# Kernel tuning notes

Measured on AMD Instinct MI355X. Metric: run time of the kernel, lower is better.

## Reference

```python
import jax, jax.numpy as jnp
import numpy as np

H = 768


def lstm_cell(x, h, c, Wih, Whh, b):
    # PyTorch LSTMCell gate order: i, f, g, o
    gates = x @ Wih.T + h @ Whh.T + b
    i, f, g, o = jnp.split(gates, 4, axis=-1)
    c = jax.nn.sigmoid(f) * c + jax.nn.sigmoid(i) * jnp.tanh(g)
    h = jax.nn.sigmoid(o) * jnp.tanh(c)
    return h, c


def run_lstm(x, Wih, Whh, b, reverse):
    B = x.shape[0]
    Hd = Whh.shape[1]
    def step(carry, xt):
        h, c = lstm_cell(xt, carry[0], carry[1], Wih, Whh, b)
        return (h, c), h
    init = (jnp.zeros((B, Hd), x.dtype), jnp.zeros((B, Hd), x.dtype))
    _, hs = jax.lax.scan(step, init, jnp.swapaxes(x, 0, 1), reverse=reverse)
    return jnp.swapaxes(hs, 0, 1)


def _forward(hidden_state, golds, lstm_Wih_f, lstm_Whh_f, lstm_b_f,
             lstm_Wih_b, lstm_Whh_b, lstm_b_b, subw_Wih, subw_Whh, subw_b,
             word_Wih, word_Whh, word_b, cls_W, cls_b):
    B, T, _ = hidden_state.shape
    dt = hidden_state.dtype
    out_f = run_lstm(hidden_state, lstm_Wih_f, lstm_Whh_f, lstm_b_f, False)
    out_b = run_lstm(hidden_state, lstm_Wih_b, lstm_Whh_b, lstm_b_b, True)
    lstm_out = jnp.concatenate([out_f, out_b], -1)  # [B, T, 2H]

    subw_map = jnp.array([1, 2, 2], dtype=jnp.int32)
    word_map = jnp.array([0, 1, 1], dtype=jnp.int32)
    bidx = jnp.arange(B)
    S1, S2 = 2 * T + 2, T + 1
    carry0 = (jnp.zeros((S1, B, H), dt), jnp.zeros((S1, B, H), dt), jnp.zeros((B,), jnp.int32),
              jnp.zeros((S2, B, H), dt), jnp.zeros((S2, B, H), dt), jnp.zeros((B,), jnp.int32))
    xs = (jnp.swapaxes(lstm_out[:, :T - 1], 0, 1),  # features for subword cell at step idx-1
          jnp.swapaxes(lstm_out[:, 1:T], 0, 1),     # features concatenated into cls at step idx
          golds[:, 1:T].T.astype(jnp.int32))

    def step(carry, x):
        sh, sc, spos, wh, wc, wpos = carry
        x_prev, x_cur, g = x
        # subword stack-LSTM: read top-of-stack state, push new state at pos+1
        h1, c1 = lstm_cell(x_prev, sh[spos, bidx], sc[spos, bidx], subw_Wih, subw_Whh, subw_b)
        sh = sh.at[spos + 1, bidx].set(h1)
        sc = sc.at[spos + 1, bidx].set(c1)
        subword = jnp.concatenate([h1, c1], -1)  # [B, 2H] input to word stack-LSTM
        # word stack-LSTM
        h2, c2 = lstm_cell(subword, wh[wpos, bidx], wc[wpos, bidx], word_Wih, word_Whh, word_b)
        wh = wh.at[wpos + 1, bidx].set(h2)
        wc = wc.at[wpos + 1, bidx].set(c2)
        out = jnp.concatenate([h2, x_cur], -1) @ cls_W.T + cls_b  # [B, 2]
        # training path: ops from gold actions
        sop = subw_map[g]
        wop = word_map[g]
        spos = jnp.where(sop == 1, spos + 1, 0)      # APP: push; SEP: clear subword stack
        wpos = jnp.where(wop == 1, wpos + 1, wpos)   # SEP: push word; APP: hold
        return (sh, sc, spos, wh, wc, wpos), out

    _, outs = jax.lax.scan(step, carry0, xs)  # [T-1, B, 2]
    pred0 = jnp.broadcast_to(jnp.asarray([-1.0, 1.0], dt), (1, B, 2))
    return jnp.swapaxes(jnp.concatenate([pred0, outs], 0), 0, 1)  # [B, T, 2]


def setup_inputs() -> dict:
    key = jax.random.key(0)
    ks = jax.random.split(key, 12)
    B, T = 64, 256
    s = 0.02
    W = lambda k, shape: jax.random.normal(k, shape, jnp.float32) * s
    return {
        "hidden_state": jax.random.normal(ks[0], (B, T, H), jnp.float32),
        "golds": jax.random.randint(ks[1], (B, T), 0, 2),
        "lstm_Wih_f": W(ks[2], (4 * H, H)), "lstm_Whh_f": W(ks[3], (4 * H, H)), "lstm_b_f": jnp.zeros((4 * H,), jnp.float32),
        "lstm_Wih_b": W(ks[4], (4 * H, H)), "lstm_Whh_b": W(ks[5], (4 * H, H)), "lstm_b_b": jnp.zeros((4 * H,), jnp.float32),
        "subw_Wih": W(ks[6], (4 * H, 2 * H)), "subw_Whh": W(ks[7], (4 * H, H)), "subw_b": jnp.zeros((4 * H,), jnp.float32),
        "word_Wih": W(ks[8], (4 * H, 2 * H)), "word_Whh": W(ks[9], (4 * H, H)), "word_b": jnp.zeros((4 * H,), jnp.float32),
        "cls_W": W(ks[10], (2, 3 * H)), "cls_b": jnp.zeros((2,), jnp.float32),
    }


def reference(hidden_state, golds, lstm_Wih_f, lstm_Whh_f, lstm_b_f,
              lstm_Wih_b, lstm_Whh_b, lstm_b_b, subw_Wih, subw_Whh, subw_b,
              word_Wih, word_Whh, word_b, cls_W, cls_b):
    return _forward(hidden_state, golds, lstm_Wih_f, lstm_Whh_f, lstm_b_f,
                    lstm_Wih_b, lstm_Whh_b, lstm_b_b, subw_Wih, subw_Whh, subw_b,
                    word_Wih, word_Whh, word_b, cls_W, cls_b)
```

## Files before the change

kernel.cpp:

```cpp
#include <hip/hip_runtime.h>
#include <hip/hip_bf16.h>

typedef __attribute__((ext_vector_type(8))) short bf16x8;
typedef __attribute__((ext_vector_type(4))) float f32x4;
typedef __attribute__((ext_vector_type(4))) unsigned u32x4;

#define HD   768
#define NB   64
#define NT   256
#define NGATE 3072
#define FPAD 32

__device__ __forceinline__ float fast_sig(float x) { return 1.f / (1.f + __expf(-x)); }
__device__ __forceinline__ float fast_tanh(float x) {
  float t = __expf(-2.f * fabsf(x));
  float r = (1.f - t) / (1.f + t);
  return x < 0.f ? -r : r;
}
__device__ __forceinline__ float bf2f(unsigned short u) {
  union { unsigned i; float f; } v; v.i = ((unsigned)u) << 16; return v.f;
}
__device__ __forceinline__ unsigned short f2bfu(float f) {
  union { __hip_bfloat16 b; unsigned short u; } c;
  c.b = __float2bfloat16(f);
  return c.u;
}
__device__ __forceinline__ unsigned pack2(float a, float b) {
  return (unsigned)f2bfu(a) | ((unsigned)f2bfu(b) << 16);
}

__device__ __forceinline__ int aload(int* p) {
  return __hip_atomic_load(p, __ATOMIC_RELAXED, __HIP_MEMORY_SCOPE_AGENT);
}
__device__ __forceinline__ void ustore(unsigned* p, unsigned v) {
  __hip_atomic_store(p, v, __ATOMIC_RELAXED, __HIP_MEMORY_SCOPE_AGENT);
}
__device__ __forceinline__ u32x4 cload16(const char* p) {
  u32x4 r;
  asm volatile("global_load_dwordx4 %0, %1, off sc0 sc1"
               : "=v"(r) : "v"(p) : "memory");
  return r;
}

__device__ __forceinline__ void arrive_flag(int* f) {
  asm volatile("s_waitcnt vmcnt(0)" ::: "memory");
  __syncthreads();
  if (threadIdx.x == 0)
    __hip_atomic_fetch_add(f, 1, __ATOMIC_RELAXED, __HIP_MEMORY_SCOPE_AGENT);
}

__device__ __forceinline__ void wait2(int* fa, int ta, int* fb, int tb) {
  int tid = threadIdx.x;
  int* p = nullptr; int tgt = 0;
  if (tid < 96)                            { p = fa + tid * FPAD;         tgt = ta; }
  else if (fb && tid >= 128 && tid < 224)  { p = fb + (tid - 128) * FPAD; tgt = tb; }
  if (p && tgt > 0) {
    int guard = 0;
    while (aload(p) < tgt) {
      __builtin_amdgcn_s_sleep(1);
      if (++guard > (1 << 17)) break;
    }
  }
  __syncthreads();
}

__device__ __forceinline__ int frag_dw(int b, int j) {
  return (((((j >> 5) * 4 + (b >> 4)) * 4 + ((j >> 3) & 3)) * 16 + (b & 15)) * 4)
         + ((j & 7) >> 1);
}

__device__ __forceinline__ int wswz(int r) {
  return ((r & 7) << 4) | (((r >> 3) & 3) << 7);
}

__device__ __forceinline__ void load_W_lds(unsigned short* Wl,
                                           const __hip_bfloat16* Wg,
                                           int n_base, int K)
{
  int chunksPerRow = (K * 2) / 16;
  int total = 32 * chunksPerRow;
  for (int idx = threadIdx.x; idx < total; idx += 256) {
    int r  = idx / chunksPerRow;
    int cb = (idx % chunksPerRow) * 16;
    bf16x8 v = *(const bf16x8*)((const char*)(Wg + (long)(n_base + r) * K) + cb);
    *(bf16x8*)((char*)Wl + (long)r * (K * 2) + (cb ^ wswz(r))) = v;
  }
}

__device__ __forceinline__ void mfma_cached(
    const __hip_bfloat16* a0p, int NIT,
    const char* w0, const char* w1, int xr0, int xr1, int kk,
    f32x4& acc0, f32x4& acc1)
{
  #pragma unroll 4
  for (int it = 0; it < NIT; ++it) {
    bf16x8 av = *(const bf16x8*)(a0p + it * 32 + kk);
    int oo = (it * 32 + kk) * 2;
    bf16x8 bv0 = *(const bf16x8*)(w0 + (oo ^ xr0));
    bf16x8 bv1 = *(const bf16x8*)(w1 + (oo ^ xr1));
    acc0 = __builtin_amdgcn_mfma_f32_16x16x32_bf16(av, bv0, acc0, 0, 0, 0);
    acc1 = __builtin_amdgcn_mfma_f32_16x16x32_bf16(av, bv1, acc1, 0, 0, 0);
  }
}

template<int CF>
__device__ __forceinline__ void mfma_frag(
    const char* Fbase, int l, int w,
    const char* w0, const char* w1, int xr0, int xr1, int kk, int kbase,
    f32x4& acc0, f32x4& acc1)
{
  const char* fp = Fbase + (size_t)(w * 64 + l) * 16;
  u32x4 st[2][12];
  #pragma unroll
  for (int i = 0; i < 12; ++i)
    st[0][i] = cload16(fp + (size_t)i * 4096);
  #pragma unroll
  for (int c = 0; c < CF / 12; ++c) {
    if (c + 1 < CF / 12) {
      #pragma unroll
      for (int i = 0; i < 12; ++i)
        st[(c + 1) & 1][i] = cload16(fp + (size_t)((c + 1) * 12 + i) * 4096);
      asm volatile("s_waitcnt vmcnt(12)" ::: "memory");
    } else {
      asm volatile("s_waitcnt vmcnt(0)" ::: "memory");
    }
    __builtin_amdgcn_sched_barrier(0);
    #pragma unroll
    for (int i = 0; i < 12; ++i) {
      int oo = ((kbase + c * 12 + i) * 32 + kk) * 2;
      bf16x8 av = __builtin_bit_cast(bf16x8, st[c & 1][i]);
      bf16x8 bv0 = *(const bf16x8*)(w0 + (oo ^ xr0));
      bf16x8 bv1 = *(const bf16x8*)(w1 + (oo ^ xr1));
      acc0 = __builtin_amdgcn_mfma_f32_16x16x32_bf16(av, bv0, acc0, 0, 0, 0);
      acc1 = __builtin_amdgcn_mfma_f32_16x16x32_bf16(av, bv1, acc1, 0, 0, 0);
    }
  }
}

__device__ __forceinline__ void pack_seg(const float* Wih, const float* Whh,
                                         __hip_bfloat16* dst, int Kih,
                                         long id0, long stride)
{
  int K = Kih + HD;
  long total = (long)NGATE * K;
  for (long idx = id0; idx < total; idx += stride) {
    int np = (int)(idx / K), k = (int)(idx % K);
    int j = np >> 2, g = np & 3;
    int n = g * HD + j;
    float v = (k < Kih) ? Wih[(long)n * Kih + k] : Whh[(long)n * HD + (k - Kih)];
    dst[idx] = __float2bfloat16(v);
  }
}

__global__ void setup_kernel(
    const float* __restrict__ x,
    const float* __restrict__ WihF, const float* __restrict__ WhhF,
    const float* __restrict__ WihB, const float* __restrict__ WhhB,
    const float* __restrict__ WihS, const float* __restrict__ WhhS,
    const float* __restrict__ WihW, const float* __restrict__ WhhW,
    __hip_bfloat16* __restrict__ X16,
    __hip_bfloat16* __restrict__ WF, __hip_bfloat16* __restrict__ WB,
    __hip_bfloat16* __restrict__ WS, __hip_bfloat16* __restrict__ WW)
{
  long id0 = (long)blockIdx.x * blockDim.x + threadIdx.x;
  long stride = (long)gridDim.x * blockDim.x;
  for (long i = id0; i < (long)NB * NT * HD; i += stride)
    X16[i] = __float2bfloat16(x[i]);
  pack_seg(WihF, WhhF, WF, 768, id0, stride);
  pack_seg(WihB, WhhB, WB, 768, id0, stride);
  pack_seg(WihS, WhhS, WS, 1536, id0, stride);
  pack_seg(WihW, WhhW, WW, 1536, id0, stride);
}

__global__ void fill_sentinel(float* out, int n, float v)
{
  int i = blockIdx.x * blockDim.x + threadIdx.x;
  if (i < n) out[i] = v;
}

__global__ __launch_bounds__(256, 1) void bilstm_persist(
    const __hip_bfloat16* __restrict__ X16,
    const __hip_bfloat16* __restrict__ WF,
    const __hip_bfloat16* __restrict__ WB,
    const float* __restrict__ bF, const float* __restrict__ bB,
    unsigned* __restrict__ H16u,
    __hip_bfloat16* __restrict__ L16,
    int* __restrict__ flags)
{
  __shared__ unsigned short Wl[32 * 1536];
  __shared__ float gl[64][33];
  int blk = blockIdx.x, dir = blk / 96, nt = blk % 96;
  load_W_lds(Wl, dir ? WB : WF, nt * 32, 1536);
  const float* bias = dir ? bB : bF;
  int* myflags = flags + dir * 96 * FPAD;
  int tid = threadIdx.x;
  unsigned* L16u = (unsigned*)L16;

  int w = tid >> 6, l = tid & 63, lr = l & 15, lh = l >> 4;
  const char* w0 = (const char*)Wl + lr * 3072;
  const char* w1 = (const char*)Wl + (16 + lr) * 3072;
  int xr0 = wswz(lr), xr1 = wswz(16 + lr);
  int kk = 8 * lh;
  int bA = 16 * w + lr;

  int e0 = tid * 2;
  int b = e0 >> 3, jj = e0 & 7;
  int j0 = nt * 8 + jj;
  float bv[2][4];
  #pragma unroll
  for (int u = 0; u < 2; ++u) {
    bv[u][0] = bias[j0 + u];          bv[u][1] = bias[HD + j0 + u];
    bv[u][2] = bias[2 * HD + j0 + u]; bv[u][3] = bias[3 * HD + j0 + u];
  }
  int fdw = frag_dw(b, j0);
  float cst[2] = {0.f, 0.f};
  __syncthreads();

  for (int s = 0; s < NT; ++s) {
    int par = s & 1;
    int t = dir ? (NT - 1 - s) : s;
    f32x4 acc0 = {0.f, 0.f, 0.f, 0.f};
    f32x4 acc1 = {0.f, 0.f, 0.f, 0.f};
    mfma_cached(X16 + (long)t * HD + (long)bA * (NT * HD), 24,
                w0, w1, xr0, xr1, kk, acc0, acc1);
    if (s > 0) wait2(myflags, s, nullptr, 0);
    mfma_frag<24>((const char*)(H16u + (long)(par * 2 + dir) * 24576),
                  l, w, w0, w1, xr0, xr1, kk, 24, acc0, acc1);
    #pragma unroll
    for (int r = 0; r < 4; ++r) {
      gl[16 * w + 4 * lh + r][lr]      = acc0[r];
      gl[16 * w + 4 * lh + r][16 + lr] = acc1[r];
    }
    __syncthreads();
    float hv[2];
    #pragma unroll
    for (int u = 0; u < 2; ++u) {
      int col = 4 * (jj + u);
      float vi = gl[b][col + 0] + bv[u][0];
      float vf = gl[b][col + 1] + bv[u][1];
      float vg = gl[b][col + 2] + bv[u][2];
      float vo = gl[b][col + 3] + bv[u][3];
      float si = fast_sig(vi), sf = fast_sig(vf), so = fast_sig(vo);
      float tg = fast_tanh(vg);
      float c = sf * cst[u] + si * tg;
      cst[u] = c;
      hv[u] = so * fast_tanh(c);
    }
    unsigned pk = pack2(hv[0], hv[1]);
    ustore(H16u + (long)((par ^ 1) * 2 + dir) * 24576 + fdw, pk);
    L16u[((long)b * NT + t) * 768 + dir * 384 + (j0 >> 1)] = pk;
    if (s < NT - 1) arrive_flag(myflags + nt * FPAD);
  }
}

__global__ __launch_bounds__(256) void clsx_kernel(
    const __hip_bfloat16* __restrict__ L16,
    const float* __restrict__ clsW, const float* __restrict__ clsb,
    float* __restrict__ out)
{
  int t = blockIdx.x;
  int tid = threadIdx.x;
  if (tid >= 128) return;
  int b = tid >> 1, o = tid & 1;
  if (t == 0) {
    out[((long)b * NT) * 2 + o] = o ? 1.f : -1.f;
    return;
  }
  const bf16x8* xp = (const bf16x8*)(L16 + ((long)b * NT + t) * 1536);
  const float* w = clsW + o * 2304 + HD;
  float s = clsb[o];
  for (int k = 0; k < 192; ++k) {
    bf16x8 v = xp[k];
    #pragma unroll
    for (int e = 0; e < 8; ++e)
      s += bf2f((unsigned short)v[e]) * w[k * 8 + e];
  }
  out[((long)b * NT + t) * 2 + o] = s;
}

__global__ __launch_bounds__(256, 1) void stack_persist(
    const __hip_bfloat16* __restrict__ L16,
    const __hip_bfloat16* __restrict__ WS,
    const __hip_bfloat16* __restrict__ WW,
    const float* __restrict__ bS, const float* __restrict__ bW,
    const int* __restrict__ golds,
    const float* __restrict__ clsW,
    unsigned* __restrict__ H1Su,
    unsigned* __restrict__ H2Su,
    unsigned* __restrict__ SUBWu,
    float* __restrict__ out,
    int* __restrict__ flags)
{
  __shared__ unsigned short Wl[32 * 2304];
  __shared__ float gl[64][33];
  int blk = blockIdx.x, role = blk / 96, nt = blk % 96;
  int* flagS = flags + 2 * 96 * FPAD;
  int* flagW = flags + 3 * 96 * FPAD;
  const float* bias = role ? bW : bS;
  load_W_lds(Wl, role ? WW : WS, nt * 32, 2304);
  int tid = threadIdx.x;

  int w = tid >> 6, l = tid & 63, lr = l & 15, lh = l >> 4;
  const char* w0 = (const char*)Wl + lr * 4608;
  const char* w1 = (const char*)Wl + (16 + lr) * 4608;
  int xr0 = wswz(lr), xr1 = wswz(16 + lr);
  int kk = 8 * lh;
  int bA = 16 * w + lr;

  int e0 = tid * 2;
  int b = e0 >> 3, jj = e0 & 7;
  int j0 = nt * 8 + jj;
  float bv[2][4];
  #pragma unroll
  for (int u = 0; u < 2; ++u) {
    bv[u][0] = bias[j0 + u];          bv[u][1] = bias[HD + j0 + u];
    bv[u][2] = bias[2 * HD + j0 + u]; bv[u][3] = bias[3 * HD + j0 + u];
  }
  const int* gp = golds + b * NT + 1;
  int fdw_h = frag_dw(b, j0);
  float cst[2] = {0.f, 0.f};
  float hreg[2] = {0.f, 0.f};
  __syncthreads();

  if (role == 0) {
    int fdw_c = frag_dw(b, 768 + j0);
    for (int s = 0; s < NT - 1; ++s) {
      f32x4 acc0 = {0.f, 0.f, 0.f, 0.f};
      f32x4 acc1 = {0.f, 0.f, 0.f, 0.f};
      mfma_cached(L16 + (long)s * 1536 + (long)bA * (NT * 1536), 48,
                  w0, w1, xr0, xr1, kk, acc0, acc1);
      wait2(flagS, s, flagW, s - 3);
      mfma_frag<24>((const char*)(H1Su + (long)(s & 1) * 24576),
                    l, w, w0, w1, xr0, xr1, kk, 48, acc0, acc1);
      #pragma unroll
      for (int r = 0; r < 4; ++r) {
        gl[16 * w + 4 * lh + r][lr]      = acc0[r];
        gl[16 * w + 4 * lh + r][16 + lr] = acc1[r];
      }
      __syncthreads();
      float h1v[2], c1v[2];
      #pragma unroll
      for (int u = 0; u < 2; ++u) {
        int col = 4 * (jj + u);
        float vi = gl[b][col + 0] + bv[u][0];
        float vf = gl[b][col + 1] + bv[u][1];
        float vg = gl[b][col + 2] + bv[u][2];
        float vo = gl[b][col + 3] + bv[u][3];
        float si = fast_sig(vi), sf = fast_sig(vf), so = fast_sig(vo);
        float tg = fast_tanh(vg);
        c1v[u] = sf * cst[u] + si * tg;
        h1v[u] = so * fast_tanh(c1v[u]);
      }
      int g = gp[s];
      bool push = (g == 0);
      unsigned pkh = pack2(h1v[0], h1v[1]);
      unsigned pkc = pack2(c1v[0], c1v[1]);
      unsigned* sb = SUBWu + (long)(s & 3) * 49152;
      ustore(sb + fdw_h, pkh);
      ustore(sb + fdw_c, pkc);
      ustore(H1Su + (long)((s + 1) & 1) * 24576 + fdw_h, push ? pkh : 0u);
      cst[0] = push ? c1v[0] : 0.f;
      cst[1] = push ? c1v[1] : 0.f;
      arrive_flag(flagS + nt * FPAD);
    }
  } else {
    float cw0[2], cw1[2];
    #pragma unroll
    for (int u = 0; u < 2; ++u) { cw0[u] = clsW[j0 + u]; cw1[u] = clsW[2304 + j0 + u]; }
    for (int s = 0; s < NT - 1; ++s) {
      wait2(flagW, s, nullptr, 0);
      f32x4 acc0 = {0.f, 0.f, 0.f, 0.f};
      f32x4 acc1 = {0.f, 0.f, 0.f, 0.f};
      mfma_frag<24>((const char*)(H2Su + (long)(s & 1) * 24576),
                    l, w, w0, w1, xr0, xr1, kk, 48, acc0, acc1);
      wait2(flagS, s + 1, nullptr, 0);
      mfma_frag<48>((const char*)(SUBWu + (long)(s & 3) * 49152),
                    l, w, w0, w1, xr0, xr1, kk, 0, acc0, acc1);
      #pragma unroll
      for (int r = 0; r < 4; ++r) {
        gl[16 * w + 4 * lh + r][lr]      = acc0[r];
        gl[16 * w + 4 * lh + r][16 + lr] = acc1[r];
      }
      __syncthreads();
      float p0 = 0.f, p1 = 0.f;
      float h2v[2], c2v[2];
      #pragma unroll
      for (int u = 0; u < 2; ++u) {
        int col = 4 * (jj + u);
        float vi = gl[b][col + 0] + bv[u][0];
        float vf = gl[b][col + 1] + bv[u][1];
        float vg = gl[b][col + 2] + bv[u][2];
        float vo = gl[b][col + 3] + bv[u][3];
        float si = fast_sig(vi), sf = fast_sig(vf), so = fast_sig(vo);
        float tg = fast_tanh(vg);
        c2v[u] = sf * cst[u] + si * tg;
        h2v[u] = so * fast_tanh(c2v[u]);
        p0 += h2v[u] * cw0[u];
        p1 += h2v[u] * cw1[u];
      }
      int g = gp[s];
      bool push = (g >= 1);
      #pragma unroll
      for (int u = 0; u < 2; ++u) {
        cst[u]  = push ? c2v[u] : cst[u];
        hreg[u] = push ? h2v[u] : hreg[u];
      }
      ustore(H2Su + (long)((s + 1) & 1) * 24576 + fdw_h, pack2(hreg[0], hreg[1]));
      p0 += __shfl_down(p0, 1); p1 += __shfl_down(p1, 1);
      p0 += __shfl_down(p0, 2); p1 += __shfl_down(p1, 2);
      if ((tid & 3) == 0) {
        int bb = tid >> 2;
        atomicAdd(&out[((long)bb * NT + s + 1) * 2 + 0], p0);
        atomicAdd(&out[((long)bb * NT + s + 1) * 2 + 1], p1);
      }
      if (s < NT - 2) arrive_flag(flagW + nt * FPAD);
    }
  }
}

extern "C" void kernel_launch(void* const* d_in, const int* in_sizes, int n_in,
                              void* d_out, int out_size, void* d_ws, size_t ws_size,
                              hipStream_t stream)
{
  const float* x     = (const float*)d_in[0];
  const int*   golds = (const int*)d_in[1];
  const float* WihF  = (const float*)d_in[2];
  const float* WhhF  = (const float*)d_in[3];
  const float* bF    = (const float*)d_in[4];
  const float* WihB  = (const float*)d_in[5];
  const float* WhhB  = (const float*)d_in[6];
  const float* bB    = (const float*)d_in[7];
  const float* WihS  = (const float*)d_in[8];
  const float* WhhS  = (const float*)d_in[9];
  const float* bS    = (const float*)d_in[10];
  const float* WihW  = (const float*)d_in[11];
  const float* WhhW  = (const float*)d_in[12];
  const float* bW    = (const float*)d_in[13];
  const float* clsW  = (const float*)d_in[14];
  const float* clsb  = (const float*)d_in[15];
  float* out = (float*)d_out;

  const size_t OFF_X16  = 0;
  const size_t OFF_WF   = 25165824;
  const size_t OFF_WB   = 34603008;
  const size_t OFF_WS   = 44040192;
  const size_t OFF_WW   = 58195968;
  const size_t OFF_L16  = 72351744;
  const size_t OFF_H16  = 122683392;
  const size_t OFF_H1S  = 123076608;
  const size_t OFF_H2S  = 123273216;
  const size_t OFF_SUBW = 123469824;
  const size_t OFF_FLG  = 124256256;
  const size_t WS_NEEDED = 124305408;

  if (ws_size < WS_NEEDED) {
    fill_sentinel<<<(out_size + 255) / 256, 256, 0, stream>>>(out, out_size, 12345.f);
    return;
  }

  char* ws = (char*)d_ws;
  __hip_bfloat16* X16  = (__hip_bfloat16*)(ws + OFF_X16);
  __hip_bfloat16* WF   = (__hip_bfloat16*)(ws + OFF_WF);
  __hip_bfloat16* WB   = (__hip_bfloat16*)(ws + OFF_WB);
  __hip_bfloat16* WSp  = (__hip_bfloat16*)(ws + OFF_WS);
  __hip_bfloat16* WWp  = (__hip_bfloat16*)(ws + OFF_WW);
  __hip_bfloat16* L16  = (__hip_bfloat16*)(ws + OFF_L16);
  unsigned*       H16u = (unsigned*)(ws + OFF_H16);
  unsigned*       H1Su = (unsigned*)(ws + OFF_H1S);
  unsigned*       H2Su = (unsigned*)(ws + OFF_H2S);
  unsigned*       SUBWu= (unsigned*)(ws + OFF_SUBW);
  int*            flags= (int*)(ws + OFF_FLG);

  setup_kernel<<<4096, 256, 0, stream>>>(x, WihF, WhhF, WihB, WhhB,
                                         WihS, WhhS, WihW, WhhW,
                                         X16, WF, WB, WSp, WWp);
  hipMemsetAsync(ws + OFF_H16, 0, WS_NEEDED - OFF_H16, stream);

  bilstm_persist<<<192, 256, 0, stream>>>(X16, WF, WB, bF, bB, H16u, L16, flags);

  clsx_kernel<<<NT, 256, 0, stream>>>(L16, clsW, clsb, out);

  stack_persist<<<192, 256, 0, stream>>>(L16, WSp, WWp, bS, bW, golds, clsW,
                                         H1Su, H2Su, SUBWu, out, flags);
}
```

Baseline: 4.056 ms.

## Overlap recurrent-state fragment loads with input-projection MFMAs and deepen load pipelining

The bidirectional LSTM and subword-cell loops now split the cached input-projection MFMA work in half. They issue all 24 coherent loads of the recurrent h fragment right after the flag wait, then run the second half of the input MFMAs while those loads are in flight. The word-cell loop issues the H2 loads before waiting on the subword flag and keeps three 12-load groups in flight with explicit vmcnt waits, instead of running two sequential double-buffered fragment passes. The classifier kernel now uses all 256 threads, with each pair splitting the dot product, and gold reads are hoisted. The cost is higher register pressure from more buffered fragments, plus reliance on hand-counted vmcnt values.

New measurement: 4.145 ms (median of 2 runs). 1.02x slower.

```diff
diff --git a/kernel.cpp b/kernel.cpp
--- a/kernel.cpp
+++ b/kernel.cpp
@@ -28,6 +28,9 @@
 __device__ __forceinline__ unsigned pack2(float a, float b) {
   return (unsigned)f2bfu(a) | ((unsigned)f2bfu(b) << 16);
 }
+
+#define VMW(N) do { asm volatile("s_waitcnt vmcnt(" #N ")" ::: "memory"); \
+                    __builtin_amdgcn_sched_barrier(0); } while (0)
 
 __device__ __forceinline__ int aload(int* p) {
   return __hip_atomic_load(p, __ATOMIC_RELAXED, __HIP_MEMORY_SCOPE_AGENT);
@@ -88,12 +91,12 @@
 }
 
 __device__ __forceinline__ void mfma_cached(
-    const __hip_bfloat16* a0p, int NIT,
+    const __hip_bfloat16* a0p, int kbase, int NIT,
     const char* w0, const char* w1, int xr0, int xr1, int kk,
     f32x4& acc0, f32x4& acc1)
 {
   #pragma unroll 4
-  for (int it = 0; it < NIT; ++it) {
+  for (int it = kbase; it < kbase + NIT; ++it) {
     bf16x8 av = *(const bf16x8*)(a0p + it * 32 + kk);
     int oo = (it * 32 + kk) * 2;
     bf16x8 bv0 = *(const bf16x8*)(w0 + (oo ^ xr0));
@@ -103,37 +106,25 @@
   }
 }
 
-template<int CF>
-__device__ __forceinline__ void mfma_frag(
-    const char* Fbase, int l, int w,
-    const char* w0, const char* w1, int xr0, int xr1, int kk, int kbase,
-    f32x4& acc0, f32x4& acc1)
-{
-  const char* fp = Fbase + (size_t)(w * 64 + l) * 16;
-  u32x4 st[2][12];
+__device__ __forceinline__ void issue12(u32x4* dst, const char* base, int c0) {
   #pragma unroll
   for (int i = 0; i < 12; ++i)
-    st[0][i] = cload16(fp + (size_t)i * 4096);
+    dst[i] = cload16(base + (size_t)(c0 + i) * 4096);
+}
+
+__device__ __forceinline__ void mfma_st12(
+    const u32x4* st, int kbase,
+    const char* w0, const char* w1, int xr0, int xr1, int kk,
+    f32x4& acc0, f32x4& acc1)
+{
   #pragma unroll
-  for (int c = 0; c < CF / 12; ++c) {
-    if (c + 1 < CF / 12) {
-      #pragma unroll
-      for (int i = 0; i < 12; ++i)
-        st[(c + 1) & 1][i] = cload16(fp + (size_t)((c + 1) * 12 + i) * 4096);
-      asm volatile("s_waitcnt vmcnt(12)" ::: "memory");
-    } else {
-      asm volatile("s_waitcnt vmcnt(0)" ::: "memory");
-    }
-    __builtin_amdgcn_sched_barrier(0);
-    #pragma unroll
-    for (int i = 0; i < 12; ++i) {
-      int oo = ((kbase + c * 12 + i) * 32 + kk) * 2;
-      bf16x8 av = __builtin_bit_cast(bf16x8, st[c & 1][i]);
-      bf16x8 bv0 = *(const bf16x8*)(w0 + (oo ^ xr0));
-      bf16x8 bv1 = *(const bf16x8*)(w1 + (oo ^ xr1));
-      acc0 = __builtin_amdgcn_mfma_f32_16x16x32_bf16(av, bv0, acc0, 0, 0, 0);
-      acc1 = __builtin_amdgcn_mfma_f32_16x16x32_bf16(av, bv1, acc1, 0, 0, 0);
-    }
+  for (int i = 0; i < 12; ++i) {
+    int oo = ((kbase + i) * 32 + kk) * 2;
+    bf16x8 av = __builtin_bit_cast(bf16x8, st[i]);
+    bf16x8 bv0 = *(const bf16x8*)(w0 + (oo ^ xr0));
+    bf16x8 bv1 = *(const bf16x8*)(w1 + (oo ^ xr1));
+    acc0 = __builtin_amdgcn_mfma_f32_16x16x32_bf16(av, bv0, acc0, 0, 0, 0);
+    acc1 = __builtin_amdgcn_mfma_f32_16x16x32_bf16(av, bv1, acc1, 0, 0, 0);
   }
 }
 
@@ -219,13 +210,20 @@
   for (int s = 0; s < NT; ++s) {
     int par = s & 1;
     int t = dir ? (NT - 1 - s) : s;
+    const __hip_bfloat16* xb = X16 + (long)t * HD + (long)bA * (NT * HD);
     f32x4 acc0 = {0.f, 0.f, 0.f, 0.f};
     f32x4 acc1 = {0.f, 0.f, 0.f, 0.f};
-    mfma_cached(X16 + (long)t * HD + (long)bA * (NT * HD), 24,
-                w0, w1, xr0, xr1, kk, acc0, acc1);
+    mfma_cached(xb, 0, 12, w0, w1, xr0, xr1, kk, acc0, acc1);
     if (s > 0) wait2(myflags, s, nullptr, 0);
-    mfma_frag<24>((const char*)(H16u + (long)(par * 2 + dir) * 24576),
-                  l, w, w0, w1, xr0, xr1, kk, 24, acc0, acc1);
+    const char* fpH = (const char*)(H16u + (long)(par * 2 + dir) * 24576)
+                      + (size_t)(w * 64 + l) * 16;
+    u32x4 hA[12], hB[12];
+    issue12(hA, fpH, 0);
+    issue12(hB, fpH, 12);
+    mfma_cached(xb, 12, 12, w0, w1, xr0, xr1, kk, acc0, acc1);
+    VMW(0);
+    mfma_st12(hA, 24, w0, w1, xr0, xr1, kk, acc0, acc1);
+    mfma_st12(hB, 36, w0, w1, xr0, xr1, kk, acc0, acc1);
     #pragma unroll
     for (int r = 0; r < 4; ++r) {
       gl[16 * w + 4 * lh + r][lr]      = acc0[r];
@@ -260,22 +258,22 @@
 {
   int t = blockIdx.x;
   int tid = threadIdx.x;
-  if (tid >= 128) return;
-  int b = tid >> 1, o = tid & 1;
+  int b = tid >> 2, o = (tid >> 1) & 1, hh = tid & 1;
   if (t == 0) {
-    out[((long)b * NT) * 2 + o] = o ? 1.f : -1.f;
+    if (hh == 0) out[((long)b * NT) * 2 + o] = o ? 1.f : -1.f;
     return;
   }
-  const bf16x8* xp = (const bf16x8*)(L16 + ((long)b * NT + t) * 1536);
-  const float* w = clsW + o * 2304 + HD;
-  float s = clsb[o];
-  for (int k = 0; k < 192; ++k) {
+  const bf16x8* xp = (const bf16x8*)(L16 + ((long)b * NT + t) * 1536 + hh * 768);
+  const float* wv = clsW + o * 2304 + HD + hh * 768;
+  float s = 0.f;
+  for (int k = 0; k < 96; ++k) {
     bf16x8 v = xp[k];
     #pragma unroll
     for (int e = 0; e < 8; ++e)
-      s += bf2f((unsigned short)v[e]) * w[k * 8 + e];
-  }
-  out[((long)b * NT + t) * 2 + o] = s;
+      s += bf2f((unsigned short)v[e]) * wv[k * 8 + e];
+  }
+  s += __shfl_down(s, 1);
+  if (hh == 0) out[((long)b * NT + t) * 2 + o] = s + clsb[o];
 }
 
 __global__ __launch_bounds__(256, 1) void stack_persist(
@@ -325,13 +323,21 @@
   if (role == 0) {
     int fdw_c = frag_dw(b, 768 + j0);
     for (int s = 0; s < NT - 1; ++s) {
+      int g = gp[s];
+      const __hip_bfloat16* lb = L16 + (long)s * 1536 + (long)bA * (NT * 1536);
       f32x4 acc0 = {0.f, 0.f, 0.f, 0.f};
       f32x4 acc1 = {0.f, 0.f, 0.f, 0.f};
-      mfma_cached(L16 + (long)s * 1536 + (long)bA * (NT * 1536), 48,
-                  w0, w1, xr0, xr1, kk, acc0, acc1);
+      mfma_cached(lb, 0, 24, w0, w1, xr0, xr1, kk, acc0, acc1);
       wait2(flagS, s, flagW, s - 3);
-      mfma_frag<24>((const char*)(H1Su + (long)(s & 1) * 24576),
-                    l, w, w0, w1, xr0, xr1, kk, 48, acc0, acc1);
+      const char* fpH1 = (const char*)(H1Su + (long)(s & 1) * 24576)
+                         + (size_t)(w * 64 + l) * 16;
+      u32x4 hA[12], hB[12];
+      issue12(hA, fpH1, 0);
+      issue12(hB, fpH1, 12);
+      mfma_cached(lb, 24, 24, w0, w1, xr0, xr1, kk, acc0, acc1);
+      VMW(0);
+      mfma_st12(hA, 48, w0, w1, xr0, xr1, kk, acc0, acc1);
+      mfma_st12(hB, 60, w0, w1, xr0, xr1, kk, acc0, acc1);
       #pragma unroll
       for (int r = 0; r < 4; ++r) {
         gl[16 * w + 4 * lh + r][lr]      = acc0[r];
@@ -351,7 +357,6 @@
         c1v[u] = sf * cst[u] + si * tg;
         h1v[u] = so * fast_tanh(c1v[u]);
       }
-      int g = gp[s];
       bool push = (g == 0);
       unsigned pkh = pack2(h1v[0], h1v[1]);
       unsigned pkc = pack2(c1v[0], c1v[1]);
@@ -368,14 +373,34 @@
     #pragma unroll
     for (int u = 0; u < 2; ++u) { cw0[u] = clsW[j0 + u]; cw1[u] = clsW[2304 + j0 + u]; }
     for (int s = 0; s < NT - 1; ++s) {
+      int g = gp[s];
       wait2(flagW, s, nullptr, 0);
+      const char* fpH = (const char*)(H2Su + (long)(s & 1) * 24576)
+                        + (size_t)(w * 64 + l) * 16;
+      const char* fpS = (const char*)(SUBWu + (long)(s & 3) * 49152)
+                        + (size_t)(w * 64 + l) * 16;
+      u32x4 sA[12], sB[12], sC[12];
+      issue12(sA, fpH, 0);
+      issue12(sB, fpH, 12);
+      wait2(flagS, s + 1, nullptr, 0);
+      issue12(sC, fpS, 0);
       f32x4 acc0 = {0.f, 0.f, 0.f, 0.f};
       f32x4 acc1 = {0.f, 0.f, 0.f, 0.f};
-      mfma_frag<24>((const char*)(H2Su + (long)(s & 1) * 24576),
-                    l, w, w0, w1, xr0, xr1, kk, 48, acc0, acc1);
-      wait2(flagS, s + 1, nullptr, 0);
-      mfma_frag<48>((const char*)(SUBWu + (long)(s & 3) * 49152),
-                    l, w, w0, w1, xr0, xr1, kk, 0, acc0, acc1);
+      VMW(24);
+      mfma_st12(sA, 48, w0, w1, xr0, xr1, kk, acc0, acc1);
+      issue12(sA, fpS, 12);
+      VMW(24);
+      mfma_st12(sB, 60, w0, w1, xr0, xr1, kk, acc0, acc1);
+      issue12(sB, fpS, 24);
+      VMW(24);
+      mfma_st12(sC, 0, w0, w1, xr0, xr1, kk, acc0, acc1);
+      issue12(sC, fpS, 36);
+      VMW(24);
+      mfma_st12(sA, 12, w0, w1, xr0, xr1, kk, acc0, acc1);
+      VMW(12);
+      mfma_st12(sB, 24, w0, w1, xr0, xr1, kk, acc0, acc1);
+      VMW(0);
+      mfma_st12(sC, 36, w0, w1, xr0, xr1, kk, acc0, acc1);
       #pragma unroll
       for (int r = 0; r < 4; ++r) {
         gl[16 * w + 4 * lh + r][lr]      = acc0[r];
@@ -398,7 +423,6 @@
         p0 += h2v[u] * cw0[u];
         p1 += h2v[u] * cw1[u];
       }
-      int g = gp[s];
       bool push = (g >= 1);
       #pragma unroll
       for (int u = 0; u < 2; ++u) {
```

## Relay word-stack recurrent fragments through per-XCD L2 staging buffers

Applied to the files above, without the earlier changes.

Word-role blocks in the stack kernel discover their XCD ID and rank. Each block then copies a slice of the shared H2/SUBW fragments from coherent memory into a per-XCD relay buffer that reuses the X16 workspace, meets the other blocks on its XCD at a barrier, and reads the full 72-chunk fragment with L2-only loads instead of system-coherent ones. This is meant to cut the cost of every block doing uncached cross-die reads each step, at the price of an extra intra-XCD barrier and copy on the critical path. Smaller changes: the subword role splits its input matmul around the flag wait so more work overlaps the wait, and clsx uses all 256 threads with a shuffle reduction.

New measurement: 4.142 ms. 2.1% more time.

```diff
diff --git a/kernel.cpp b/kernel.cpp
--- a/kernel.cpp
+++ b/kernel.cpp
@@ -29,15 +29,27 @@
   return (unsigned)f2bfu(a) | ((unsigned)f2bfu(b) << 16);
 }
 
+#define VMW(N) do { asm volatile("s_waitcnt vmcnt(" #N ")" ::: "memory"); \
+                    __builtin_amdgcn_sched_barrier(0); } while (0)
+
 __device__ __forceinline__ int aload(int* p) {
   return __hip_atomic_load(p, __ATOMIC_RELAXED, __HIP_MEMORY_SCOPE_AGENT);
 }
 __device__ __forceinline__ void ustore(unsigned* p, unsigned v) {
   __hip_atomic_store(p, v, __ATOMIC_RELAXED, __HIP_MEMORY_SCOPE_AGENT);
+}
+__device__ __forceinline__ int aadd_ret(int* p) {
+  return __hip_atomic_fetch_add(p, 1, __ATOMIC_RELAXED, __HIP_MEMORY_SCOPE_AGENT);
 }
 __device__ __forceinline__ u32x4 cload16(const char* p) {
   u32x4 r;
   asm volatile("global_load_dwordx4 %0, %1, off sc0 sc1"
+               : "=v"(r) : "v"(p) : "memory");
+  return r;
+}
+__device__ __forceinline__ u32x4 l2load16(const char* p) {
+  u32x4 r;
+  asm volatile("global_load_dwordx4 %0, %1, off sc0"
                : "=v"(r) : "v"(p) : "memory");
   return r;
 }
@@ -88,12 +100,12 @@
 }
 
 __device__ __forceinline__ void mfma_cached(
-    const __hip_bfloat16* a0p, int NIT,
+    const __hip_bfloat16* a0p, int kbase, int NIT,
     const char* w0, const char* w1, int xr0, int xr1, int kk,
     f32x4& acc0, f32x4& acc1)
 {
   #pragma unroll 4
-  for (int it = 0; it < NIT; ++it) {
+  for (int it = kbase; it < kbase + NIT; ++it) {
     bf16x8 av = *(const bf16x8*)(a0p + it * 32 + kk);
     int oo = (it * 32 + kk) * 2;
     bf16x8 bv0 = *(const bf16x8*)(w0 + (oo ^ xr0));
@@ -103,7 +115,7 @@
   }
 }
 
-template<int CF>
+template<int CF, bool L2ONLY>
 __device__ __forceinline__ void mfma_frag(
     const char* Fbase, int l, int w,
     const char* w0, const char* w1, int xr0, int xr1, int kk, int kbase,
@@ -113,13 +125,15 @@
   u32x4 st[2][12];
   #pragma unroll
   for (int i = 0; i < 12; ++i)
-    st[0][i] = cload16(fp + (size_t)i * 4096);
+    st[0][i] = L2ONLY ? l2load16(fp + (size_t)i * 4096)
+                      : cload16(fp + (size_t)i * 4096);
   #pragma unroll
   for (int c = 0; c < CF / 12; ++c) {
     if (c + 1 < CF / 12) {
       #pragma unroll
       for (int i = 0; i < 12; ++i)
-        st[(c + 1) & 1][i] = cload16(fp + (size_t)((c + 1) * 12 + i) * 4096);
+        st[(c + 1) & 1][i] = L2ONLY ? l2load16(fp + (size_t)((c + 1) * 12 + i) * 4096)
+                                    : cload16(fp + (size_t)((c + 1) * 12 + i) * 4096);
       asm volatile("s_waitcnt vmcnt(12)" ::: "memory");
     } else {
       asm volatile("s_waitcnt vmcnt(0)" ::: "memory");
@@ -221,11 +235,11 @@
     int t = dir ? (NT - 1 - s) : s;
     f32x4 acc0 = {0.f, 0.f, 0.f, 0.f};
     f32x4 acc1 = {0.f, 0.f, 0.f, 0.f};
-    mfma_cached(X16 + (long)t * HD + (long)bA * (NT * HD), 24,
+    mfma_cached(X16 + (long)t * HD + (long)bA * (NT * HD), 0, 24,
                 w0, w1, xr0, xr1, kk, acc0, acc1);
     if (s > 0) wait2(myflags, s, nullptr, 0);
-    mfma_frag<24>((const char*)(H16u + (long)(par * 2 + dir) * 24576),
-                  l, w, w0, w1, xr0, xr1, kk, 24, acc0, acc1);
+    mfma_frag<24, false>((const char*)(H16u + (long)(par * 2 + dir) * 24576),
+                         l, w, w0, w1, xr0, xr1, kk, 24, acc0, acc1);
     #pragma unroll
     for (int r = 0; r < 4; ++r) {
       gl[16 * w + 4 * lh + r][lr]      = acc0[r];
@@ -260,22 +274,22 @@
 {
   int t = blockIdx.x;
   int tid = threadIdx.x;
-  if (tid >= 128) return;
-  int b = tid >> 1, o = tid & 1;
+  int b = tid >> 2, o = (tid >> 1) & 1, hh = tid & 1;
   if (t == 0) {
-    out[((long)b * NT) * 2 + o] = o ? 1.f : -1.f;
+    if (hh == 0) out[((long)b * NT) * 2 + o] = o ? 1.f : -1.f;
     return;
   }
-  const bf16x8* xp = (const bf16x8*)(L16 + ((long)b * NT + t) * 1536);
-  const float* w = clsW + o * 2304 + HD;
-  float s = clsb[o];
-  for (int k = 0; k < 192; ++k) {
+  const bf16x8* xp = (const bf16x8*)(L16 + ((long)b * NT + t) * 1536 + hh * 768);
+  const float* wv = clsW + o * 2304 + HD + hh * 768;
+  float s = 0.f;
+  for (int k = 0; k < 96; ++k) {
     bf16x8 v = xp[k];
     #pragma unroll
     for (int e = 0; e < 8; ++e)
-      s += bf2f((unsigned short)v[e]) * w[k * 8 + e];
-  }
-  out[((long)b * NT + t) * 2 + o] = s;
+      s += bf2f((unsigned short)v[e]) * wv[k * 8 + e];
+  }
+  s += __shfl_down(s, 1);
+  if (hh == 0) out[((long)b * NT + t) * 2 + o] = s + clsb[o];
 }
 
 __global__ __launch_bounds__(256, 1) void stack_persist(
@@ -288,14 +302,19 @@
     unsigned* __restrict__ H1Su,
     unsigned* __restrict__ H2Su,
     unsigned* __restrict__ SUBWu,
+    unsigned* __restrict__ relay,
     float* __restrict__ out,
     int* __restrict__ flags)
 {
   __shared__ unsigned short Wl[32 * 2304];
   __shared__ float gl[64][33];
+  __shared__ int shx[3];
   int blk = blockIdx.x, role = blk / 96, nt = blk % 96;
   int* flagS = flags + 2 * 96 * FPAD;
   int* flagW = flags + 3 * 96 * FPAD;
+  int* flagR = flags + 4 * 96 * FPAD;
+  int* xreg  = flags + 5 * 96 * FPAD;
+  int* xdone = xreg + 16 * 32;
   const float* bias = role ? bW : bS;
   load_W_lds(Wl, role ? WW : WS, nt * 32, 2304);
   int tid = threadIdx.x;
@@ -325,13 +344,15 @@
   if (role == 0) {
     int fdw_c = frag_dw(b, 768 + j0);
     for (int s = 0; s < NT - 1; ++s) {
+      int g = gp[s];
+      const __hip_bfloat16* lb = L16 + (long)s * 1536 + (long)bA * (NT * 1536);
       f32x4 acc0 = {0.f, 0.f, 0.f, 0.f};
       f32x4 acc1 = {0.f, 0.f, 0.f, 0.f};
-      mfma_cached(L16 + (long)s * 1536 + (long)bA * (NT * 1536), 48,
-                  w0, w1, xr0, xr1, kk, acc0, acc1);
+      mfma_cached(lb, 0, 24, w0, w1, xr0, xr1, kk, acc0, acc1);
       wait2(flagS, s, flagW, s - 3);
-      mfma_frag<24>((const char*)(H1Su + (long)(s & 1) * 24576),
-                    l, w, w0, w1, xr0, xr1, kk, 48, acc0, acc1);
+      mfma_cached(lb, 24, 24, w0, w1, xr0, xr1, kk, acc0, acc1);
+      mfma_frag<24, false>((const char*)(H1Su + (long)(s & 1) * 24576),
+                           l, w, w0, w1, xr0, xr1, kk, 48, acc0, acc1);
       #pragma unroll
       for (int r = 0; r < 4; ++r) {
         gl[16 * w + 4 * lh + r][lr]      = acc0[r];
@@ -351,7 +372,6 @@
         c1v[u] = sf * cst[u] + si * tg;
         h1v[u] = so * fast_tanh(c1v[u]);
       }
-      int g = gp[s];
       bool push = (g == 0);
       unsigned pkh = pack2(h1v[0], h1v[1]);
       unsigned pkc = pack2(c1v[0], c1v[1]);
@@ -364,18 +384,72 @@
       arrive_flag(flagS + nt * FPAD);
     }
   } else {
+    if (tid == 0) {
+      unsigned xid;
+      asm volatile("s_getreg_b32 %0, hwreg(HW_REG_XCC_ID)" : "=s"(xid));
+      xid &= 15;
+      shx[0] = (int)xid;
+      shx[1] = aadd_ret(xreg + xid * 32);
+      __hip_atomic_fetch_add(flagR + nt * FPAD, 1, __ATOMIC_RELAXED,
+                             __HIP_MEMORY_SCOPE_AGENT);
+    }
+    __syncthreads();
+    wait2(flagR, 1, nullptr, 0);
+    if (tid == 0) shx[2] = aload(xreg + shx[0] * 32);
+    __syncthreads();
+    int xcd = shx[0], rank = shx[1], cnt = shx[2];
+    char* rslot0 = (char*)(relay + (size_t)xcd * 2 * 73728);
+    int* mydone = xdone + xcd * 32;
+    int off_thr = ((w * 64 + l) * 16);
+
     float cw0[2], cw1[2];
     #pragma unroll
     for (int u = 0; u < 2; ++u) { cw0[u] = clsW[j0 + u]; cw1[u] = clsW[2304 + j0 + u]; }
+
     for (int s = 0; s < NT - 1; ++s) {
+      int g = gp[s];
       wait2(flagW, s, nullptr, 0);
+      char* rslot = rslot0 + (size_t)(s & 1) * 294912;
+      const char* srcH = (const char*)(H2Su + (long)(s & 1) * 24576);
+      const char* srcS = (const char*)(SUBWu + (long)(s & 3) * 49152);
+      u32x4 sv[9]; int itv[9];
+      #pragma unroll
+      for (int i = 0; i < 9; ++i) {
+        int it = rank + i * cnt;
+        itv[i] = (it < 72) ? it : 99;
+        if (itv[i] >= 48 && itv[i] < 72)
+          sv[i] = cload16(srcH + (size_t)(itv[i] - 48) * 4096 + off_thr);
+      }
+      wait2(flagS, s + 1, nullptr, 0);
+      #pragma unroll
+      for (int i = 0; i < 9; ++i)
+        if (itv[i] < 48)
+          sv[i] = cload16(srcS + (size_t)itv[i] * 4096 + off_thr);
+      VMW(0);
+      #pragma unroll
+      for (int i = 0; i < 9; ++i)
+        if (itv[i] < 72)
+          *(u32x4*)(rslot + (size_t)itv[i] * 4096 + off_thr) = sv[i];
+      for (int it = rank + 9 * cnt; it < 72; it += cnt) {
+        u32x4 v = (it >= 48) ? cload16(srcH + (size_t)(it - 48) * 4096 + off_thr)
+                             : cload16(srcS + (size_t)it * 4096 + off_thr);
+        VMW(0);
+        *(u32x4*)(rslot + (size_t)it * 4096 + off_thr) = v;
+      }
+      asm volatile("s_waitcnt vmcnt(0)" ::: "memory");
+      __syncthreads();
+      if (tid == 0) {
+        __hip_atomic_fetch_add(mydone, 1, __ATOMIC_RELAXED, __HIP_MEMORY_SCOPE_AGENT);
+        int guard = 0, tgtd = cnt * (s + 1);
+        while (aload(mydone) < tgtd) {
+          __builtin_amdgcn_s_sleep(1);
+          if (++guard > (1 << 17)) break;
+        }
+      }
+      __syncthreads();
       f32x4 acc0 = {0.f, 0.f, 0.f, 0.f};
       f32x4 acc1 = {0.f, 0.f, 0.f, 0.f};
-      mfma_frag<24>((const char*)(H2Su + (long)(s & 1) * 24576),
-                    l, w, w0, w1, xr0, xr1, kk, 48, acc0, acc1);
-      wait2(flagS, s + 1, nullptr, 0);
-      mfma_frag<48>((const char*)(SUBWu + (long)(s & 3) * 49152),
-                    l, w, w0, w1, xr0, xr1, kk, 0, acc0, acc1);
+      mfma_frag<72, true>(rslot, l, w, w0, w1, xr0, xr1, kk, 0, acc0, acc1);
       #pragma unroll
       for (int r = 0; r < 4; ++r) {
         gl[16 * w + 4 * lh + r][lr]      = acc0[r];
@@ -398,7 +472,6 @@
         p0 += h2v[u] * cw0[u];
         p1 += h2v[u] * cw1[u];
       }
-      int g = gp[s];
       bool push = (g >= 1);
       #pragma unroll
       for (int u = 0; u < 2; ++u) {
@@ -451,7 +524,7 @@
   const size_t OFF_H2S  = 123273216;
   const size_t OFF_SUBW = 123469824;
   const size_t OFF_FLG  = 124256256;
-  const size_t WS_NEEDED = 124305408;
+  const size_t WS_NEEDED = 124321792;
 
   if (ws_size < WS_NEEDED) {
     fill_sentinel<<<(out_size + 255) / 256, 256, 0, stream>>>(out, out_size, 12345.f);
@@ -469,6 +542,7 @@
   unsigned*       H1Su = (unsigned*)(ws + OFF_H1S);
   unsigned*       H2Su = (unsigned*)(ws + OFF_H2S);
   unsigned*       SUBWu= (unsigned*)(ws + OFF_SUBW);
+  unsigned*       relay= (unsigned*)(ws + OFF_X16);
   int*            flags= (int*)(ws + OFF_FLG);
 
   setup_kernel<<<4096, 256, 0, stream>>>(x, WihF, WhhF, WihB, WhhB,
@@ -481,5 +555,5 @@
   clsx_kernel<<<NT, 256, 0, stream>>>(L16, clsW, clsb, out);
 
   stack_persist<<<192, 256, 0, stream>>>(L16, WSp, WWp, bS, bW, golds, clsW,
-                                         H1Su, H2Su, SUBWu, out, flags);
-}
+                                         H1Su, H2Su, SUBWu, relay, out, flags);
+}
```
